# Performance work log

Measured on AMD Instinct MI355X. Metric: run time of the kernel, lower is better.

The kernel has to match this reference:

```python
import jax, jax.numpy as jnp
import numpy as np

DECAY = 0.1  # P['decay']


def setup_inputs() -> dict:
    key = jax.random.key(0)
    k0, k1, k2, k3, k4 = jax.random.split(key, 5)
    N, B, T = 512, 64, 1024
    hidden_0 = jax.random.normal(k0, (N,), dtype=jnp.float32)
    Batch_Input = jax.random.normal(k1, (B, T, N), dtype=jnp.float32)
    # scale recurrent weight ~1/sqrt(N) so the leaky-tanh dynamics stay bounded
    W = jax.random.normal(k2, (N, N), dtype=jnp.float32) / np.sqrt(N).astype(np.float32)
    Gw = jax.random.normal(k3, (2, N), dtype=jnp.float32)
    Gb = jax.random.normal(k4, (2,), dtype=jnp.float32)
    return {"hidden_0": hidden_0, "Batch_Input": Batch_Input, "W": W, "Gw": Gw, "Gb": Gb}


def reference(hidden_0, Batch_Input, W, Gw, Gb):
    B, T, N = Batch_Input.shape
    h0 = jnp.broadcast_to(hidden_0[None, :], (B, N))  # repeat over batch
    xs = jnp.swapaxes(Batch_Input, 0, 1)  # [T, B, N] for scan over time

    def step(h, x):
        # h_new = (1-d)*h + d*(tanh(h) @ W^T + x)   (einsum 'ab,cb->ca')
        h_new = (1.0 - DECAY) * h + DECAY * (jnp.tanh(h) @ W.T + x)
        return h_new, jnp.tanh(h_new)

    _, hidden_t = jax.lax.scan(step, h0, xs)  # hidden_t: [T, B, N]
    geometry = hidden_t @ Gw.T + Gb  # [T, B, 2]
    return jnp.swapaxes(hidden_t, 0, 1), jnp.swapaxes(geometry, 0, 1)
```

## Files before the change

### kernel.cpp

```cpp
#include <hip/hip_runtime.h>
#include <hip/hip_fp16.h>
#include <cmath>

#define RN 512
#define RT 1024
#define RB 64
#define SMEM_BYTES 86016

typedef _Float16 half2v __attribute__((ext_vector_type(2)));

__device__ __forceinline__ float fast_tanh(float x) {
    float e = __expf(2.0f * x);
    return 1.0f - 2.0f / (e + 1.0f);
}
__device__ __forceinline__ unsigned pack2(float a, float b) {
    return (unsigned)__half_as_ushort(__float2half(a)) |
           ((unsigned)__half_as_ushort(__float2half(b)) << 16);
}
__device__ __forceinline__ unsigned pkrtz(float a, float b) {
    auto h = __builtin_amdgcn_cvt_pkrtz(a, b);
    return __builtin_bit_cast(unsigned, h);
}
__device__ __forceinline__ float dot2(unsigned wa, unsigned tb, float acc) {
    half2v a = __builtin_bit_cast(half2v, wa);
    half2v b = __builtin_bit_cast(half2v, tb);
    return __builtin_amdgcn_fdot2(a, b, acc, false);
}
template <int CTRL>
__device__ __forceinline__ float dpp_add(float x) {
    int p = __builtin_amdgcn_update_dpp(0, __float_as_int(x), CTRL, 0xf, 0xf, true);
    return x + __int_as_float(p);
}
__device__ __forceinline__ float red16(float x) {
    x = dpp_add<0xB1>(x);
    x = dpp_add<0x4E>(x);
    x = dpp_add<0x141>(x);
    x = dpp_add<0x140>(x);
    return x;
}
#define D2Q(acc, wq, tq) \
    acc = dot2((wq).x, (tq).x, acc); acc = dot2((wq).y, (tq).y, acc); \
    acc = dot2((wq).z, (tq).z, acc); acc = dot2((wq).w, (tq).w, acc);

#define PIN4(v) asm volatile("" : "+v"((v).x), "+v"((v).y), "+v"((v).z), "+v"((v).w));

#define LOADB(bb) { \
    const int b_ = (part + (bb)) & 3; \
    w##bb##_0 = wsrc[(b_ * 4 + 0) * 512]; PIN4(w##bb##_0) \
    w##bb##_1 = wsrc[(b_ * 4 + 1) * 512]; PIN4(w##bb##_1) \
    w##bb##_2 = wsrc[(b_ * 4 + 2) * 512]; PIN4(w##bb##_2) \
    w##bb##_3 = wsrc[(b_ * 4 + 3) * 512]; PIN4(w##bb##_3) }

#define DOTB(bb, tv) \
    D2Q(acc0, w##bb##_0, tv) D2Q(acc1, w##bb##_1, tv) \
    D2Q(acc2, w##bb##_2, tv) D2Q(acc3, w##bb##_3, tv)

__global__ void __launch_bounds__(512, 1) rnn_step_kernel(
    const float* __restrict__ h0,
    const float* __restrict__ X,
    const uint4* __restrict__ Wpk,
    const float* __restrict__ tanh0,
    float* __restrict__ outH,
    unsigned* __restrict__ ctr,
    unsigned* __restrict__ xcdctr)
{
    extern __shared__ unsigned char smem[];
    unsigned* ownpk = (unsigned*)smem;
    int*      bc    = (int*)(smem + 256);
    unsigned* lctr  = (unsigned*)(smem + 264);

    const int tid = threadIdx.x;
    if (tid == 0) {
        unsigned xcd;
        asm volatile("s_getreg_b32 %0, hwreg(HW_REG_XCC_ID)" : "=s"(xcd));
        xcd &= 7u;
        unsigned rank = __hip_atomic_fetch_add(&xcdctr[xcd], 1u,
                            __ATOMIC_RELAXED, __HIP_MEMORY_SCOPE_AGENT) & 31u;
        int slot = (int)(xcd * 32u + rank);
        bc[0] = slot >> 2;
        bc[1] = slot & 3;
        *lctr = 0u;
    }
    __syncthreads();
    const int batch = bc[0], part = bc[1];

    uint4 w0_0, w0_1, w0_2, w0_3;
    uint4 w1_0, w1_1, w1_2, w1_3;
    uint4 w2_0, w2_1, w2_2, w2_3;
    uint4 w3_0, w3_1, w3_2, w3_3;
    {
        const uint4* wsrc = Wpk + part * 8192 + tid;
        LOADB(0) LOADB(1) LOADB(2) LOADB(3)
    }

    const int rg = tid >> 4;
    const int kc = tid & 15;
    const int row0 = part * 128 + rg * 4;

    float4 h = {0, 0, 0, 0};
    float4 xv = {0, 0, 0, 0};
    if (kc == 0) {
        h = *reinterpret_cast<const float4*>(h0 + row0);
        float t0 = tanhf(h.x), t1 = tanhf(h.y), t2 = tanhf(h.z), t3 = tanhf(h.w);
        ownpk[2 * rg]     = pack2(t0, t1);
        ownpk[2 * rg + 1] = pack2(t2, t3);
        xv = *reinterpret_cast<const float4*>(&X[(size_t)batch * RT * RN + row0]);
    }

    unsigned* gctr = ctr + batch * 32;
    __syncthreads();

    #pragma unroll 1
    for (int t = 0; t < RT; ++t) {
        float4 xn = {0, 0, 0, 0};
        if (kc == 0) {
            const int tn = (t + 1 < RT) ? t + 1 : t;
            xn = *reinterpret_cast<const float4*>(&X[((size_t)batch * RT + tn) * RN + row0]);
        }

        float acc0 = 0.f, acc1 = 0.f, acc2 = 0.f, acc3 = 0.f;
        {
            uint4 th = *reinterpret_cast<const uint4*>(&ownpk[4 * kc]);
            DOTB(0, th)
        }

        if (tid == 0 && t > 0) {
            const unsigned tgt = 4u * (unsigned)t;
            while (__hip_atomic_load(gctr, __ATOMIC_RELAXED,
                                     __HIP_MEMORY_SCOPE_AGENT) < tgt)
                __builtin_amdgcn_s_sleep(1);
        }
        __syncthreads();

        const float* srcR = (t == 0) ? tanh0
            : &outH[((size_t)batch * RT + (t - 1)) * RN];
        {
            const int b1 = (part + 1) & 3;
            const int ko = b1 * 128 + kc * 8;
            float4 f0 = *reinterpret_cast<const float4*>(srcR + ko);
            float4 f1 = *reinterpret_cast<const float4*>(srcR + ko + 4);
            uint4 tv = make_uint4(pkrtz(f0.x, f0.y), pkrtz(f0.z, f0.w),
                                  pkrtz(f1.x, f1.y), pkrtz(f1.z, f1.w));
            DOTB(1, tv)
        }
        {
            const int b2 = (part + 2) & 3;
            const int ko = b2 * 128 + kc * 8;
            float4 f0 = *reinterpret_cast<const float4*>(srcR + ko);
            float4 f1 = *reinterpret_cast<const float4*>(srcR + ko + 4);
            uint4 tv = make_uint4(pkrtz(f0.x, f0.y), pkrtz(f0.z, f0.w),
                                  pkrtz(f1.x, f1.y), pkrtz(f1.z, f1.w));
            DOTB(2, tv)
        }
        {
            const int b3 = (part + 3) & 3;
            const int ko = b3 * 128 + kc * 8;
            float4 f0 = *reinterpret_cast<const float4*>(srcR + ko);
            float4 f1 = *reinterpret_cast<const float4*>(srcR + ko + 4);
            uint4 tv = make_uint4(pkrtz(f0.x, f0.y), pkrtz(f0.z, f0.w),
                                  pkrtz(f1.x, f1.y), pkrtz(f1.z, f1.w));
            DOTB(3, tv)
        }

        acc0 = red16(acc0); acc1 = red16(acc1);
        acc2 = red16(acc2); acc3 = red16(acc3);

        if (kc == 0) {
            h.x = 0.9f * h.x + 0.1f * (acc0 + xv.x);
            h.y = 0.9f * h.y + 0.1f * (acc1 + xv.y);
            h.z = 0.9f * h.z + 0.1f * (acc2 + xv.z);
            h.w = 0.9f * h.w + 0.1f * (acc3 + xv.w);
            float t0 = fast_tanh(h.x), t1 = fast_tanh(h.y);
            float t2 = fast_tanh(h.z), t3 = fast_tanh(h.w);
            *reinterpret_cast<float4*>(&outH[((size_t)batch * RT + t) * RN + row0]) =
                make_float4(t0, t1, t2, t3);
            ownpk[2 * rg]     = pack2(t0, t1);
            ownpk[2 * rg + 1] = pack2(t2, t3);
        }

        asm volatile("s_waitcnt vmcnt(0)" ::: "memory");
        if ((tid & 63) == 0) {
            unsigned a = __hip_atomic_fetch_add(lctr, 1u, __ATOMIC_RELAXED,
                                                __HIP_MEMORY_SCOPE_WORKGROUP);
            if ((a & 7u) == 7u)
                __hip_atomic_fetch_add(gctr, 1u, __ATOMIC_RELAXED,
                                       __HIP_MEMORY_SCOPE_AGENT);
        }
        __syncthreads();
        xv = xn;
    }
}

__global__ void pack_w(const float* __restrict__ W, uint4* __restrict__ Wpk)
{
    int o = blockIdx.x * blockDim.x + threadIdx.x;
    if (o >= 32768) return;
    int part = o >> 13;
    int b    = (o >> 11) & 3;
    int i    = (o >> 9) & 3;
    int tid  = o & 511;
    int row  = part * 128 + (tid >> 4) * 4 + i;
    int k0   = b * 128 + (tid & 15) * 8;
    const float* s = W + (size_t)row * RN + k0;
    uint4 v;
    v.x = pack2(s[0], s[1]); v.y = pack2(s[2], s[3]);
    v.z = pack2(s[4], s[5]); v.w = pack2(s[6], s[7]);
    Wpk[o] = v;
}

__global__ void geom_kernel(const float* __restrict__ hid,
                            const float* __restrict__ Gw,
                            const float* __restrict__ Gb,
                            float* __restrict__ geo)
{
    const int wid  = (blockIdx.x * blockDim.x + threadIdx.x) >> 6;
    const int lane = threadIdx.x & 63;
    if (wid >= RB * RT) return;
    const float* rowp = hid + (size_t)wid * RN;
    float g0 = 0.f, g1 = 0.f;
    #pragma unroll
    for (int j = 0; j < 8; ++j) {
        float v = rowp[lane + 64 * j];
        g0 = fmaf(v, Gw[lane + 64 * j], g0);
        g1 = fmaf(v, Gw[RN + lane + 64 * j], g1);
    }
    #pragma unroll
    for (int m = 32; m >= 1; m >>= 1) {
        g0 += __shfl_xor(g0, m);
        g1 += __shfl_xor(g1, m);
    }
    if (lane == 0) {
        geo[(size_t)wid * 2]     = g0 + Gb[0];
        geo[(size_t)wid * 2 + 1] = g1 + Gb[1];
    }
}

__global__ void init_misc(const float* __restrict__ h0,
                          float* __restrict__ tanh0,
                          unsigned* __restrict__ ctr,
                          unsigned* __restrict__ xcdctr)
{
    int i = blockIdx.x * blockDim.x + threadIdx.x;
    if (i < RN) tanh0[i] = tanhf(h0[i]);
    if (i < RB * 32) ctr[i] = 0u;
    if (i < 8) xcdctr[i] = 0u;
}

extern "C" void kernel_launch(void* const* d_in, const int* in_sizes, int n_in,
                              void* d_out, int out_size, void* d_ws, size_t ws_size,
                              hipStream_t stream)
{
    const float* h0 = (const float*)d_in[0];
    const float* X  = (const float*)d_in[1];
    const float* W  = (const float*)d_in[2];
    const float* Gw = (const float*)d_in[3];
    const float* Gb = (const float*)d_in[4];

    float* outH = (float*)d_out;
    float* geo  = outH + (size_t)RB * RT * RN;

    float*    tanh0  = (float*)d_ws;
    unsigned* ctr    = (unsigned*)d_ws + RN;
    unsigned* xcdctr = ctr + RB * 32;
    uint4*    Wpk    = (uint4*)(((uintptr_t)(xcdctr + 8) + 63) & ~(uintptr_t)63);

    (void)hipFuncSetAttribute((const void*)rnn_step_kernel,
                              hipFuncAttributeMaxDynamicSharedMemorySize, SMEM_BYTES);

    pack_w<<<64, 512, 0, stream>>>(W, Wpk);
    init_misc<<<8, 512, 0, stream>>>(h0, tanh0, ctr, xcdctr);

    void* kargs[] = { (void*)&h0, (void*)&X, (void*)&Wpk, (void*)&tanh0,
                      (void*)&outH, (void*)&ctr, (void*)&xcdctr };
    (void)hipLaunchCooperativeKernel(rnn_step_kernel, dim3(256), dim3(512),
                                     kargs, SMEM_BYTES, stream);

    geom_kernel<<<(RB * RT * 64 + 255) / 256, 256, 0, stream>>>(outH, Gw, Gb, geo);
}
```

Baseline: 1.865 ms.

## Exchange packed fp16 tanh state between blocks and defer fp32 output stores

Blocks now exchange the per-step tanh state as packed fp16 pairs in a separate workspace buffer instead of reading fp32 outH and converting it. This halves the bytes on the cross-block critical path and drops the conversion work. The fp32 outH store and the next-step X load move after the counter increment, so they leave the synchronisation-critical vmcnt wait. The cost is extra workspace (B*T*256 words) and an additional global write per step.

```diff
diff --git a/kernel.cpp b/kernel.cpp
--- a/kernel.cpp
+++ b/kernel.cpp
@@ -16,10 +16,6 @@
 __device__ __forceinline__ unsigned pack2(float a, float b) {
     return (unsigned)__half_as_ushort(__float2half(a)) |
            ((unsigned)__half_as_ushort(__float2half(b)) << 16);
-}
-__device__ __forceinline__ unsigned pkrtz(float a, float b) {
-    auto h = __builtin_amdgcn_cvt_pkrtz(a, b);
-    return __builtin_bit_cast(unsigned, h);
 }
 __device__ __forceinline__ float dot2(unsigned wa, unsigned tb, float acc) {
     half2v a = __builtin_bit_cast(half2v, wa);
@@ -59,8 +55,9 @@
     const float* __restrict__ h0,
     const float* __restrict__ X,
     const uint4* __restrict__ Wpk,
-    const float* __restrict__ tanh0,
+    const unsigned* __restrict__ tanh0pk,
     float* __restrict__ outH,
+    unsigned* __restrict__ exP,
     unsigned* __restrict__ ctr,
     unsigned* __restrict__ xcdctr)
 {
@@ -112,12 +109,6 @@
 
     #pragma unroll 1
     for (int t = 0; t < RT; ++t) {
-        float4 xn = {0, 0, 0, 0};
-        if (kc == 0) {
-            const int tn = (t + 1 < RT) ? t + 1 : t;
-            xn = *reinterpret_cast<const float4*>(&X[((size_t)batch * RT + tn) * RN + row0]);
-        }
-
         float acc0 = 0.f, acc1 = 0.f, acc2 = 0.f, acc3 = 0.f;
         {
             uint4 th = *reinterpret_cast<const uint4*>(&ownpk[4 * kc]);
@@ -132,50 +123,41 @@
         }
         __syncthreads();
 
-        const float* srcR = (t == 0) ? tanh0
-            : &outH[((size_t)batch * RT + (t - 1)) * RN];
+        const unsigned* srcP = (t == 0) ? tanh0pk
+            : (exP + ((size_t)batch * RT + (t - 1)) * 256);
         {
             const int b1 = (part + 1) & 3;
-            const int ko = b1 * 128 + kc * 8;
-            float4 f0 = *reinterpret_cast<const float4*>(srcR + ko);
-            float4 f1 = *reinterpret_cast<const float4*>(srcR + ko + 4);
-            uint4 tv = make_uint4(pkrtz(f0.x, f0.y), pkrtz(f0.z, f0.w),
-                                  pkrtz(f1.x, f1.y), pkrtz(f1.z, f1.w));
+            uint4 tv = *reinterpret_cast<const uint4*>(srcP + b1 * 64 + 4 * kc);
             DOTB(1, tv)
         }
         {
             const int b2 = (part + 2) & 3;
-            const int ko = b2 * 128 + kc * 8;
-            float4 f0 = *reinterpret_cast<const float4*>(srcR + ko);
-            float4 f1 = *reinterpret_cast<const float4*>(srcR + ko + 4);
-            uint4 tv = make_uint4(pkrtz(f0.x, f0.y), pkrtz(f0.z, f0.w),
-                                  pkrtz(f1.x, f1.y), pkrtz(f1.z, f1.w));
+            uint4 tv = *reinterpret_cast<const uint4*>(srcP + b2 * 64 + 4 * kc);
             DOTB(2, tv)
         }
         {
             const int b3 = (part + 3) & 3;
-            const int ko = b3 * 128 + kc * 8;
-            float4 f0 = *reinterpret_cast<const float4*>(srcR + ko);
-            float4 f1 = *reinterpret_cast<const float4*>(srcR + ko + 4);
-            uint4 tv = make_uint4(pkrtz(f0.x, f0.y), pkrtz(f0.z, f0.w),
-                                  pkrtz(f1.x, f1.y), pkrtz(f1.z, f1.w));
+            uint4 tv = *reinterpret_cast<const uint4*>(srcP + b3 * 64 + 4 * kc);
             DOTB(3, tv)
         }
 
         acc0 = red16(acc0); acc1 = red16(acc1);
         acc2 = red16(acc2); acc3 = red16(acc3);
 
+        float t0 = 0.f, t1 = 0.f, t2 = 0.f, t3 = 0.f;
         if (kc == 0) {
             h.x = 0.9f * h.x + 0.1f * (acc0 + xv.x);
             h.y = 0.9f * h.y + 0.1f * (acc1 + xv.y);
             h.z = 0.9f * h.z + 0.1f * (acc2 + xv.z);
             h.w = 0.9f * h.w + 0.1f * (acc3 + xv.w);
-            float t0 = fast_tanh(h.x), t1 = fast_tanh(h.y);
-            float t2 = fast_tanh(h.z), t3 = fast_tanh(h.w);
-            *reinterpret_cast<float4*>(&outH[((size_t)batch * RT + t) * RN + row0]) =
-                make_float4(t0, t1, t2, t3);
-            ownpk[2 * rg]     = pack2(t0, t1);
-            ownpk[2 * rg + 1] = pack2(t2, t3);
+            t0 = fast_tanh(h.x); t1 = fast_tanh(h.y);
+            t2 = fast_tanh(h.z); t3 = fast_tanh(h.w);
+            const unsigned u0 = pack2(t0, t1), u1 = pack2(t2, t3);
+            *reinterpret_cast<uint2*>(
+                exP + ((size_t)batch * RT + t) * 256 + part * 64 + 2 * rg) =
+                make_uint2(u0, u1);
+            ownpk[2 * rg]     = u0;
+            ownpk[2 * rg + 1] = u1;
         }
 
         asm volatile("s_waitcnt vmcnt(0)" ::: "memory");
@@ -186,8 +168,14 @@
                 __hip_atomic_fetch_add(gctr, 1u, __ATOMIC_RELAXED,
                                        __HIP_MEMORY_SCOPE_AGENT);
         }
+
+        if (kc == 0) {
+            *reinterpret_cast<float4*>(&outH[((size_t)batch * RT + t) * RN + row0]) =
+                make_float4(t0, t1, t2, t3);
+            const int tn = (t + 1 < RT) ? t + 1 : t;
+            xv = *reinterpret_cast<const float4*>(&X[((size_t)batch * RT + tn) * RN + row0]);
+        }
         __syncthreads();
-        xv = xn;
     }
 }
 
@@ -236,12 +224,12 @@
 }
 
 __global__ void init_misc(const float* __restrict__ h0,
-                          float* __restrict__ tanh0,
+                          unsigned* __restrict__ tanh0pk,
                           unsigned* __restrict__ ctr,
                           unsigned* __restrict__ xcdctr)
 {
     int i = blockIdx.x * blockDim.x + threadIdx.x;
-    if (i < RN) tanh0[i] = tanhf(h0[i]);
+    if (i < 256) tanh0pk[i] = pack2(tanhf(h0[2 * i]), tanhf(h0[2 * i + 1]));
     if (i < RB * 32) ctr[i] = 0u;
     if (i < 8) xcdctr[i] = 0u;
 }
@@ -259,19 +247,20 @@
     float* outH = (float*)d_out;
     float* geo  = outH + (size_t)RB * RT * RN;
 
-    float*    tanh0  = (float*)d_ws;
-    unsigned* ctr    = (unsigned*)d_ws + RN;
-    unsigned* xcdctr = ctr + RB * 32;
-    uint4*    Wpk    = (uint4*)(((uintptr_t)(xcdctr + 8) + 63) & ~(uintptr_t)63);
+    unsigned* exP     = (unsigned*)d_ws;
+    unsigned* tanh0pk = exP + (size_t)RB * RT * 256;
+    unsigned* ctr     = tanh0pk + 256;
+    unsigned* xcdctr  = ctr + RB * 32;
+    uint4*    Wpk     = (uint4*)(((uintptr_t)(xcdctr + 8) + 63) & ~(uintptr_t)63);
 
     (void)hipFuncSetAttribute((const void*)rnn_step_kernel,
                               hipFuncAttributeMaxDynamicSharedMemorySize, SMEM_BYTES);
 
     pack_w<<<64, 512, 0, stream>>>(W, Wpk);
-    init_misc<<<8, 512, 0, stream>>>(h0, tanh0, ctr, xcdctr);
-
-    void* kargs[] = { (void*)&h0, (void*)&X, (void*)&Wpk, (void*)&tanh0,
-                      (void*)&outH, (void*)&ctr, (void*)&xcdctr };
+    init_misc<<<8, 512, 0, stream>>>(h0, tanh0pk, ctr, xcdctr);
+
+    void* kargs[] = { (void*)&h0, (void*)&X, (void*)&Wpk, (void*)&tanh0pk,
+                      (void*)&outH, (void*)&exP, (void*)&ctr, (void*)&xcdctr };
     (void)hipLaunchCooperativeKernel(rnn_step_kernel, dim3(256), dim3(512),
                                      kargs, SMEM_BYTES, stream);
 
```

Measured after the change: 2.215 ms. 18.8% more time.
